# Kernel optimization log

Hardware: AMD Instinct MI355X
Metric: run time of the kernel (lower is better)

Reference implementation:

```python
import jax, jax.numpy as jnp
import numpy as np

B, T, D = 4, 2048, 1024
RANK, FACTOR, SUB = 8, 64, 4
S = 4 * SUB  # 16


def construct_hamilton(A):
    # A: [rank, 4, sub, sub] -> [rank, 4*sub, 4*sub]
    r, i, j, k = A[:, 0], A[:, 1], A[:, 2], A[:, 3]
    return jnp.concatenate([
        jnp.concatenate([r, -i, -j, -k], axis=2),
        jnp.concatenate([i, r, -k, j], axis=2),
        jnp.concatenate([j, k, r, -i], axis=2),
        jnp.concatenate([k, -j, i, r], axis=2),
    ], axis=1)


def setup_inputs() -> dict:
    key = jax.random.key(0)
    k1, k2, k3 = jax.random.split(key, 3)
    x = jax.random.normal(k1, (B, T, D), dtype=jnp.float32)
    A = jax.random.normal(k2, (RANK, 4, SUB, SUB), dtype=jnp.float32)
    # orthogonal-ish init with (r+1)^-0.5 scaling, like the torch init
    fB = jax.random.normal(k3, (RANK, FACTOR, FACTOR), dtype=jnp.float32)
    q, _ = jnp.linalg.qr(fB)
    scale = (jnp.arange(RANK, dtype=jnp.float32) + 1.0) ** -0.5
    factors_B = q * scale[:, None, None]
    bias = jnp.zeros((D,), dtype=jnp.float32)
    return {"x": x, "A": A, "factors_B": factors_B, "bias": bias}


def reference(x, A, factors_B, bias):
    Bb, Tt, Dd = x.shape
    x_flat = x.reshape(-1, S, FACTOR)          # [N, s, i]
    H = construct_hamilton(A)                   # [r, k, s]
    wav = jnp.einsum('nsi,rji->rnsj', x_flat, factors_B)  # [r, N, s, j]
    out = jnp.einsum('rnsj,rks->nkj', wav, H)   # [N, k, j]
    return out.reshape(Bb, Tt, Dd) + bias
```

## Files before the change

kernel.cpp:

```cpp
#include <hip/hip_runtime.h>
#include <stdint.h>

#define RANKS 8
#define MDIM 8192
#define KDIM 1024
#define NDIM 1024
#define BM 256
#define BN 128
#define BK 64
#define NT (KDIM / BK)
#define THREADS 512

typedef __bf16 bf16x8 __attribute__((ext_vector_type(8)));
typedef float f32x4 __attribute__((ext_vector_type(4)));

__device__ __forceinline__ unsigned short f2bf(float f) {
  union { float f; uint32_t u; } v; v.f = f;
  uint32_t u = v.u;
  u += 0x7FFFu + ((u >> 16) & 1u);
  return (unsigned short)(u >> 16);
}

__constant__ int   c_comp[4][4] = {{0,1,2,3},{1,0,3,2},{2,3,0,1},{3,2,1,0}};
__constant__ float c_sign[4][4] = {{1.f,-1.f,-1.f,-1.f},
                                   {1.f, 1.f,-1.f, 1.f},
                                   {1.f, 1.f, 1.f,-1.f},
                                   {1.f,-1.f, 1.f, 1.f}};

__global__ void build_W(const float* __restrict__ A, const float* __restrict__ fB,
                        unsigned short* __restrict__ W) {
  int idx = blockIdx.x * 256 + threadIdx.x;
  int p  = idx >> 8;
  int q4 = (idx & 255) << 2;
  int k = p >> 6, j = p & 63;
  int kb = k >> 2, ks = k & 3;
  int s = q4 >> 6;
  int sb = s >> 2, ss = s & 3;
  int   comp = c_comp[kb][sb];
  float sgn  = c_sign[kb][sb];
  float o0 = 0.f, o1 = 0.f, o2 = 0.f, o3 = 0.f;
  int i0 = q4 & 63;
#pragma unroll
  for (int r = 0; r < RANKS; ++r) {
    float h = sgn * A[r * 64 + comp * 16 + ks * 4 + ss];
    const float* fb = fB + r * 4096 + j * 64 + i0;
    o0 += h * fb[0]; o1 += h * fb[1]; o2 += h * fb[2]; o3 += h * fb[3];
  }
  ushort4 st;
  st.x = f2bf(o0); st.y = f2bf(o1); st.z = f2bf(o2); st.w = f2bf(o3);
  *reinterpret_cast<ushort4*>(W + (size_t)p * KDIM + q4) = st;
}

__global__ void cvt_x(const float* __restrict__ x, unsigned short* __restrict__ xb) {
  int b = blockIdx.x;
  int i = (b & 7) * 512 + (b >> 3);
  size_t base = ((size_t)i * 256 + threadIdx.x) * 8;
  float4 a = *reinterpret_cast<const float4*>(x + base);
  float4 c = *reinterpret_cast<const float4*>(x + base + 4);
  bf16x8 v;
  v[0] = (__bf16)a.x; v[1] = (__bf16)a.y; v[2] = (__bf16)a.z; v[3] = (__bf16)a.w;
  v[4] = (__bf16)c.x; v[5] = (__bf16)c.y; v[6] = (__bf16)c.z; v[7] = (__bf16)c.w;
  *reinterpret_cast<bf16x8*>(xb + base) = v;
}

__device__ __forceinline__ void gload16(const unsigned short* g, unsigned short* l) {
  __builtin_amdgcn_global_load_lds(
      (const __attribute__((address_space(1))) unsigned int*)(uintptr_t)g,
      (__attribute__((address_space(3))) unsigned int*)(uintptr_t)l,
      16, 0, 0);
}

#define SWZ(r, cbyte) (((r) * 128) + ((cbyte) ^ (((r) & 7) << 4)))

__global__ __launch_bounds__(THREADS, 2) void gemm_ham(
    const unsigned short* __restrict__ Xb, const unsigned short* __restrict__ W,
    const float* __restrict__ bias, float* __restrict__ out) {
  __shared__ unsigned short Asm_[3][BM * BK];
  __shared__ unsigned short Bsm_[3][BN * BK];

  const int tid  = threadIdx.x;
  const int lane = tid & 63;
  const int wid  = tid >> 6;
  const int wr   = wid >> 1;
  const int wc   = wid & 1;
  const int rb   = lane & 15;
  const int qtr  = lane >> 4;

  const int flat = blockIdx.x;
  const int xg = flat & 7, ig = flat >> 3;
  const int bx = xg * 4 + (ig >> 3);
  const int by = ig & 7;
  const int row0 = bx * BM;
  const int col0 = by * BN;

  f32x4 acc[4][4];
  f32x4 zero = {0.f, 0.f, 0.f, 0.f};
#pragma unroll
  for (int m = 0; m < 4; ++m)
#pragma unroll
    for (int n = 0; n < 4; ++n) acc[m][n] = zero;

  auto stageA = [&](int kt, int slot, int g) {
    int id = g * 512 + tid;
    int r = id >> 3, ct = id & 7;
    gload16(Xb + (size_t)(row0 + r) * KDIM + kt * BK + ((ct ^ (r & 7)) << 3),
            &Asm_[slot][id * 8]);
  };
  auto stageB = [&](int kt, int slot, int g) {
    int id = g * 512 + tid;
    int r = id >> 3, ct = id & 7;
    gload16(W + (size_t)(col0 + r) * KDIM + kt * BK + ((ct ^ (r & 7)) << 3),
            &Bsm_[slot][id * 8]);
  };

  auto phase = [&](const char* Ab, const char* Bb, int kk, int t2, int slot2,
                   bool dl, int half) {
    bf16x8 af[4], bfr[4];
    const int cb = qtr * 16 + kk * 64;
#pragma unroll
    for (int m = 0; m < 4; ++m)
      af[m] = *reinterpret_cast<const bf16x8*>(Ab + SWZ(wr * 64 + m * 16 + rb, cb));
#pragma unroll
    for (int n = 0; n < 4; ++n)
      bfr[n] = *reinterpret_cast<const bf16x8*>(Bb + SWZ(wc * 64 + n * 16 + rb, cb));
    if (dl) {
      if (half == 0) { stageA(t2, slot2, 0); stageA(t2, slot2, 1); stageB(t2, slot2, 0); }
      else           { stageA(t2, slot2, 2); stageA(t2, slot2, 3); stageB(t2, slot2, 1); }
    }
    __builtin_amdgcn_sched_barrier(0);
    __builtin_amdgcn_s_barrier();
    asm volatile("s_waitcnt lgkmcnt(0)" ::: "memory");
    __builtin_amdgcn_sched_barrier(0);
    __builtin_amdgcn_s_setprio(1);
#pragma unroll
    for (int m = 0; m < 4; ++m)
#pragma unroll
      for (int n = 0; n < 4; ++n)
        acc[m][n] = __builtin_amdgcn_mfma_f32_16x16x32_bf16(af[m], bfr[n], acc[m][n], 0, 0, 0);
    __builtin_amdgcn_s_setprio(0);
    __builtin_amdgcn_sched_barrier(0);
  };

  stageA(0, 0, 0); stageA(0, 0, 1); stageA(0, 0, 2); stageA(0, 0, 3);
  stageB(0, 0, 0); stageB(0, 0, 1);
  stageA(1, 1, 0); stageA(1, 1, 1); stageA(1, 1, 2); stageA(1, 1, 3);
  stageB(1, 1, 0); stageB(1, 1, 1);
  asm volatile("s_waitcnt vmcnt(6)" ::: "memory");
  __builtin_amdgcn_sched_barrier(0);
  __builtin_amdgcn_s_barrier();
  __builtin_amdgcn_sched_barrier(0);

  int sc = 0;
#pragma unroll 1
  for (int t = 0; t < NT; ++t) {
    const char* Ab = reinterpret_cast<const char*>(&Asm_[sc][0]);
    const char* Bb = reinterpret_cast<const char*>(&Bsm_[sc][0]);
    int slot2 = sc + 2; if (slot2 >= 3) slot2 -= 3;
    const bool dl = (t + 2 < NT);
    phase(Ab, Bb, 0, t + 2, slot2, dl, 0);
    __builtin_amdgcn_s_barrier();
    phase(Ab, Bb, 1, t + 2, slot2, dl, 1);
    if (t < NT - 1) {
      if (t < NT - 2) asm volatile("s_waitcnt vmcnt(6)" ::: "memory");
      else            asm volatile("s_waitcnt vmcnt(0)" ::: "memory");
      __builtin_amdgcn_sched_barrier(0);
      __builtin_amdgcn_s_barrier();
      __builtin_amdgcn_sched_barrier(0);
    }
    sc = sc + 1; if (sc >= 3) sc -= 3;
  }

  const int crow = row0 + wr * 64 + qtr * 4;
  const int ccol = col0 + wc * 64 + rb;
#pragma unroll
  for (int n = 0; n < 4; ++n) {
    int c = ccol + n * 16;
    float bv = bias[c];
#pragma unroll
    for (int m = 0; m < 4; ++m)
#pragma unroll
      for (int v = 0; v < 4; ++v)
        out[(size_t)(crow + m * 16 + v) * NDIM + c] = acc[m][n][v] + bv;
  }
}

__global__ void fallback_kernel(const float* __restrict__ x, const float* __restrict__ A,
                                const float* __restrict__ fB, const float* __restrict__ bias,
                                float* __restrict__ out) {
  __shared__ float xrow[1024];
  const int n = blockIdx.x;
  const int tid = threadIdx.x;
  for (int t = tid; t < 1024; t += 256) xrow[t] = x[(size_t)n * 1024 + t];
  __syncthreads();
  for (int pp = 0; pp < 4; ++pp) {
    int p = pp * 256 + tid;
    int k = p >> 6, j = p & 63;
    int kb = k >> 2, ks = k & 3;
    float accv = 0.f;
    for (int s = 0; s < 16; ++s) {
      int sb = s >> 2, ss = s & 3;
      int comp = c_comp[kb][sb];
      float sgn = c_sign[kb][sb];
      float hA[RANKS];
#pragma unroll
      for (int r = 0; r < RANKS; ++r) hA[r] = sgn * A[r * 64 + comp * 16 + ks * 4 + ss];
      for (int i = 0; i < 64; ++i) {
        float w = 0.f;
#pragma unroll
        for (int r = 0; r < RANKS; ++r) w += hA[r] * fB[r * 4096 + j * 64 + i];
        accv += xrow[s * 64 + i] * w;
      }
    }
    out[(size_t)n * 1024 + p] = accv + bias[p];
  }
}

extern "C" void kernel_launch(void* const* d_in, const int* in_sizes, int n_in,
                              void* d_out, int out_size, void* d_ws, size_t ws_size,
                              hipStream_t stream) {
  const float* x    = (const float*)d_in[0];
  const float* A    = (const float*)d_in[1];
  const float* fB   = (const float*)d_in[2];
  const float* bias = (const float*)d_in[3];
  float* out = (float*)d_out;

  const size_t needW = (size_t)NDIM * KDIM * sizeof(unsigned short);
  const size_t needX = (size_t)MDIM * KDIM * sizeof(unsigned short);
  if (ws_size >= needW + needX) {
    unsigned short* W  = (unsigned short*)d_ws;
    unsigned short* Xb = W + (size_t)NDIM * KDIM;
    build_W<<<dim3(1024), dim3(256), 0, stream>>>(A, fB, W);
    cvt_x<<<dim3(4096), dim3(256), 0, stream>>>(x, Xb);
    gemm_ham<<<dim3((MDIM / BM) * (NDIM / BN)), dim3(THREADS), 0, stream>>>(Xb, W, bias, out);
  } else {
    fallback_kernel<<<dim3(MDIM), dim3(256), 0, stream>>>(x, A, fB, bias, out);
  }
}
```

Measured before the change: 40.52 us.

## Fuse fp32-to-bf16 conversion of x into GEMM and shrink tiles

Removes the separate cvt_x pass by streaming fp32 x directly into LDS and converting to bf16 when loading MFMA fragments. This saves a full write and reread of a bf16 copy of x and one kernel launch. To fit fp32 tiles in LDS, the block tile becomes 128x128 with K-step 32 and 256 threads, and the two-phase interleaved prefetch schedule becomes one prefetch per iteration. In exchange it doubles the A-tile LDS traffic, adds conversion ALU work in the inner loop, and halves MFMA work per barrier.

```diff
diff --git a/kernel.cpp b/kernel.cpp
--- a/kernel.cpp
+++ b/kernel.cpp
@@ -5,11 +5,11 @@
 #define MDIM 8192
 #define KDIM 1024
 #define NDIM 1024
-#define BM 256
+#define BM 128
 #define BN 128
-#define BK 64
+#define BK 32
 #define NT (KDIM / BK)
-#define THREADS 512
+#define THREADS 256
 
 typedef __bf16 bf16x8 __attribute__((ext_vector_type(8)));
 typedef float f32x4 __attribute__((ext_vector_type(4)));
@@ -51,31 +51,17 @@
   *reinterpret_cast<ushort4*>(W + (size_t)p * KDIM + q4) = st;
 }
 
-__global__ void cvt_x(const float* __restrict__ x, unsigned short* __restrict__ xb) {
-  int b = blockIdx.x;
-  int i = (b & 7) * 512 + (b >> 3);
-  size_t base = ((size_t)i * 256 + threadIdx.x) * 8;
-  float4 a = *reinterpret_cast<const float4*>(x + base);
-  float4 c = *reinterpret_cast<const float4*>(x + base + 4);
-  bf16x8 v;
-  v[0] = (__bf16)a.x; v[1] = (__bf16)a.y; v[2] = (__bf16)a.z; v[3] = (__bf16)a.w;
-  v[4] = (__bf16)c.x; v[5] = (__bf16)c.y; v[6] = (__bf16)c.z; v[7] = (__bf16)c.w;
-  *reinterpret_cast<bf16x8*>(xb + base) = v;
-}
-
-__device__ __forceinline__ void gload16(const unsigned short* g, unsigned short* l) {
+__device__ __forceinline__ void gload16(const void* g, void* l) {
   __builtin_amdgcn_global_load_lds(
       (const __attribute__((address_space(1))) unsigned int*)(uintptr_t)g,
       (__attribute__((address_space(3))) unsigned int*)(uintptr_t)l,
       16, 0, 0);
 }
 
-#define SWZ(r, cbyte) (((r) * 128) + ((cbyte) ^ (((r) & 7) << 4)))
-
 __global__ __launch_bounds__(THREADS, 2) void gemm_ham(
-    const unsigned short* __restrict__ Xb, const unsigned short* __restrict__ W,
+    const float* __restrict__ x, const unsigned short* __restrict__ W,
     const float* __restrict__ bias, float* __restrict__ out) {
-  __shared__ unsigned short Asm_[3][BM * BK];
+  __shared__ float          Asm_[3][BM * BK];
   __shared__ unsigned short Bsm_[3][BN * BK];
 
   const int tid  = threadIdx.x;
@@ -88,7 +74,7 @@
 
   const int flat = blockIdx.x;
   const int xg = flat & 7, ig = flat >> 3;
-  const int bx = xg * 4 + (ig >> 3);
+  const int bx = xg * 8 + (ig >> 3);
   const int by = ig & 7;
   const int row0 = bx * BM;
   const int col0 = by * BN;
@@ -100,51 +86,27 @@
 #pragma unroll
     for (int n = 0; n < 4; ++n) acc[m][n] = zero;
 
-  auto stageA = [&](int kt, int slot, int g) {
-    int id = g * 512 + tid;
-    int r = id >> 3, ct = id & 7;
-    gload16(Xb + (size_t)(row0 + r) * KDIM + kt * BK + ((ct ^ (r & 7)) << 3),
-            &Asm_[slot][id * 8]);
+  auto stageA = [&](int kt, int slot) {
+#pragma unroll
+    for (int g = 0; g < 4; ++g) {
+      int id = g * 256 + tid;
+      int r = id >> 3, ct = id & 7;
+      gload16(x + (size_t)(row0 + r) * KDIM + kt * BK + ((ct ^ (r & 7)) << 2),
+              &Asm_[slot][id * 4]);
+    }
   };
-  auto stageB = [&](int kt, int slot, int g) {
-    int id = g * 512 + tid;
-    int r = id >> 3, ct = id & 7;
-    gload16(W + (size_t)(col0 + r) * KDIM + kt * BK + ((ct ^ (r & 7)) << 3),
-            &Bsm_[slot][id * 8]);
+  auto stageB = [&](int kt, int slot) {
+#pragma unroll
+    for (int g = 0; g < 2; ++g) {
+      int id = g * 256 + tid;
+      int r = id >> 2, ct = id & 3;
+      gload16(W + (size_t)(col0 + r) * KDIM + kt * BK + (ct << 3),
+              &Bsm_[slot][id * 8]);
+    }
   };
 
-  auto phase = [&](const char* Ab, const char* Bb, int kk, int t2, int slot2,
-                   bool dl, int half) {
-    bf16x8 af[4], bfr[4];
-    const int cb = qtr * 16 + kk * 64;
-#pragma unroll
-    for (int m = 0; m < 4; ++m)
-      af[m] = *reinterpret_cast<const bf16x8*>(Ab + SWZ(wr * 64 + m * 16 + rb, cb));
-#pragma unroll
-    for (int n = 0; n < 4; ++n)
-      bfr[n] = *reinterpret_cast<const bf16x8*>(Bb + SWZ(wc * 64 + n * 16 + rb, cb));
-    if (dl) {
-      if (half == 0) { stageA(t2, slot2, 0); stageA(t2, slot2, 1); stageB(t2, slot2, 0); }
-      else           { stageA(t2, slot2, 2); stageA(t2, slot2, 3); stageB(t2, slot2, 1); }
-    }
-    __builtin_amdgcn_sched_barrier(0);
-    __builtin_amdgcn_s_barrier();
-    asm volatile("s_waitcnt lgkmcnt(0)" ::: "memory");
-    __builtin_amdgcn_sched_barrier(0);
-    __builtin_amdgcn_s_setprio(1);
-#pragma unroll
-    for (int m = 0; m < 4; ++m)
-#pragma unroll
-      for (int n = 0; n < 4; ++n)
-        acc[m][n] = __builtin_amdgcn_mfma_f32_16x16x32_bf16(af[m], bfr[n], acc[m][n], 0, 0, 0);
-    __builtin_amdgcn_s_setprio(0);
-    __builtin_amdgcn_sched_barrier(0);
-  };
-
-  stageA(0, 0, 0); stageA(0, 0, 1); stageA(0, 0, 2); stageA(0, 0, 3);
-  stageB(0, 0, 0); stageB(0, 0, 1);
-  stageA(1, 1, 0); stageA(1, 1, 1); stageA(1, 1, 2); stageA(1, 1, 3);
-  stageB(1, 1, 0); stageB(1, 1, 1);
+  stageA(0, 0); stageB(0, 0);
+  stageA(1, 1); stageB(1, 1);
   asm volatile("s_waitcnt vmcnt(6)" ::: "memory");
   __builtin_amdgcn_sched_barrier(0);
   __builtin_amdgcn_s_barrier();
@@ -153,13 +115,38 @@
   int sc = 0;
 #pragma unroll 1
   for (int t = 0; t < NT; ++t) {
+    int s2 = sc + 2; if (s2 >= 3) s2 -= 3;
+    if (t + 2 < NT) { stageA(t + 2, s2); stageB(t + 2, s2); }
+
     const char* Ab = reinterpret_cast<const char*>(&Asm_[sc][0]);
     const char* Bb = reinterpret_cast<const char*>(&Bsm_[sc][0]);
-    int slot2 = sc + 2; if (slot2 >= 3) slot2 -= 3;
-    const bool dl = (t + 2 < NT);
-    phase(Ab, Bb, 0, t + 2, slot2, dl, 0);
-    __builtin_amdgcn_s_barrier();
-    phase(Ab, Bb, 1, t + 2, slot2, dl, 1);
+    bf16x8 af[4], bfr[4];
+#pragma unroll
+    for (int m = 0; m < 4; ++m) {
+      int r = wr * 64 + m * 16 + rb;
+      int u0 = (qtr * 2)     ^ (r & 7);
+      int u1 = (qtr * 2 + 1) ^ (r & 7);
+      f32x4 lo = *reinterpret_cast<const f32x4*>(Ab + r * 128 + (u0 << 4));
+      f32x4 hi = *reinterpret_cast<const f32x4*>(Ab + r * 128 + (u1 << 4));
+      bf16x8 v;
+      v[0] = (__bf16)lo[0]; v[1] = (__bf16)lo[1]; v[2] = (__bf16)lo[2]; v[3] = (__bf16)lo[3];
+      v[4] = (__bf16)hi[0]; v[5] = (__bf16)hi[1]; v[6] = (__bf16)hi[2]; v[7] = (__bf16)hi[3];
+      af[m] = v;
+    }
+#pragma unroll
+    for (int n = 0; n < 4; ++n) {
+      int r = wc * 64 + n * 16 + rb;
+      bfr[n] = *reinterpret_cast<const bf16x8*>(Bb + r * 64 + qtr * 16);
+    }
+
+    __builtin_amdgcn_s_setprio(1);
+#pragma unroll
+    for (int m = 0; m < 4; ++m)
+#pragma unroll
+      for (int n = 0; n < 4; ++n)
+        acc[m][n] = __builtin_amdgcn_mfma_f32_16x16x32_bf16(af[m], bfr[n], acc[m][n], 0, 0, 0);
+    __builtin_amdgcn_s_setprio(0);
+
     if (t < NT - 1) {
       if (t < NT - 2) asm volatile("s_waitcnt vmcnt(6)" ::: "memory");
       else            asm volatile("s_waitcnt vmcnt(0)" ::: "memory");
@@ -225,13 +212,10 @@
   float* out = (float*)d_out;
 
   const size_t needW = (size_t)NDIM * KDIM * sizeof(unsigned short);
-  const size_t needX = (size_t)MDIM * KDIM * sizeof(unsigned short);
-  if (ws_size >= needW + needX) {
-    unsigned short* W  = (unsigned short*)d_ws;
-    unsigned short* Xb = W + (size_t)NDIM * KDIM;
+  if (ws_size >= needW) {
+    unsigned short* W = (unsigned short*)d_ws;
     build_W<<<dim3(1024), dim3(256), 0, stream>>>(A, fB, W);
-    cvt_x<<<dim3(4096), dim3(256), 0, stream>>>(x, Xb);
-    gemm_ham<<<dim3((MDIM / BM) * (NDIM / BN)), dim3(THREADS), 0, stream>>>(Xb, W, bias, out);
+    gemm_ham<<<dim3((MDIM / BM) * (NDIM / BN)), dim3(THREADS), 0, stream>>>(x, W, bias, out);
   } else {
     fallback_kernel<<<dim3(MDIM), dim3(256), 0, stream>>>(x, A, fB, bias, out);
   }
```

Result: faster. 37.27 us (-8.0%).
